# Performance work log

Hardware: AMD Instinct MI355X
Metric: run time of the kernel (lower is better)

The kernel has to match this reference:

```python
import jax, jax.numpy as jnp
import numpy as np

B, T, C = 2, 2048, 1024
H = 16
D = C // H  # head_dim = 64


def setup_inputs() -> dict:
    key = jax.random.key(0)
    k1, k2, k3, k4, k5 = jax.random.split(key, 5)
    s = 0.02
    return {
        "x": jax.random.normal(k1, (B, T, C), dtype=jnp.float32),
        "w_qkv": jax.random.normal(k2, (C, 3 * C), dtype=jnp.float32) * s,
        "b_qkv": jnp.zeros((3 * C,), dtype=jnp.float32),
        "w_proj": jax.random.normal(k3, (C, C), dtype=jnp.float32) * s,
        "b_proj": jnp.zeros((C,), dtype=jnp.float32),
    }


def reference(x, w_qkv, b_qkv, w_proj, b_proj):
    b, t, c = x.shape
    qkv = x @ w_qkv + b_qkv                      # [B,T,3C]
    q, k, v = jnp.split(qkv, 3, axis=-1)
    # [B,T,C] -> [B,H,T,D]
    q = q.reshape(b, t, H, D).transpose(0, 2, 1, 3)
    k = k.reshape(b, t, H, D).transpose(0, 2, 1, 3)
    v = v.reshape(b, t, H, D).transpose(0, 2, 1, 3)
    att = jnp.einsum("bhqd,bhkd->bhqk", q, k) / jnp.sqrt(jnp.float32(D))
    causal = jnp.tril(jnp.ones((t, t), dtype=bool))  # True where allowed
    att = jnp.where(causal, att, -jnp.inf)
    att = jax.nn.softmax(att, axis=-1)
    out = jnp.einsum("bhqk,bhkd->bhqd", att, v)      # [B,H,T,D]
    out = out.transpose(0, 2, 1, 3).reshape(b, t, c)
    return out @ w_proj + b_proj
```

## Files before the change

### kernel.cpp

```cpp
#include <hip/hip_runtime.h>
#include <hip/hip_bf16.h>
#include <math.h>
#include <stdint.h>

#define B_ 2
#define T_ 2048
#define C_ 1024
#define H_ 16
#define D_ 64

typedef __attribute__((ext_vector_type(8))) short bf16x8;
typedef __attribute__((ext_vector_type(4))) float f32x4;

__device__ inline short f2bf(float f) {
  __hip_bfloat16 h = __float2bfloat16(f);
  return *(short*)&h;
}

__device__ inline void async16(const void* g, void* l) {
  __builtin_amdgcn_global_load_lds(
      (const __attribute__((address_space(1))) uint32_t*)g,
      (__attribute__((address_space(3))) uint32_t*)l, 16, 0, 0);
}


__global__ __launch_bounds__(256) void prep(
    const float* __restrict__ X, const float* __restrict__ Wq,
    const float* __restrict__ Wp, short* __restrict__ Xb,
    short* __restrict__ Wqt, short* __restrict__ Wpt) {
  const int tid = threadIdx.x;
  const int blk = blockIdx.x;
  __shared__ short Ts[64][68];

  if (blk < 512) {
    int t = blk * 256 + tid;
    int m = t >> 5, g = t & 31;
    const float* src = X + (size_t)m * C_ + g * 32;
    short* dst = Xb + (size_t)m * C_ + g * 32;
    int xv = (m >> 1) & 3;
    short out[32];
#pragma unroll
    for (int ch = 0; ch < 4; ++ch) {
      int sc = ch ^ xv;
#pragma unroll
      for (int e = 0; e < 8; e += 4) {
        float4 v = *(const float4*)(src + sc * 8 + e);
        out[ch * 8 + e + 0] = f2bf(v.x);
        out[ch * 8 + e + 1] = f2bf(v.y);
        out[ch * 8 + e + 2] = f2bf(v.z);
        out[ch * 8 + e + 3] = f2bf(v.w);
      }
    }
#pragma unroll
    for (int q = 0; q < 4; ++q) *(uint4*)(dst + q * 8) = *(uint4*)(out + q * 8);
    return;
  }

  const float* W;
  short* Wt;
  int N, n0, k0;
  if (blk < 1280) {
    int i = blk - 512;
    W = Wq; Wt = Wqt; N = 3 * C_;
    n0 = (i % 48) * 64; k0 = (i / 48) * 64;
  } else {
    int i = blk - 1280;
    W = Wp; Wt = Wpt; N = C_;
    n0 = (i & 15) * 64; k0 = (i >> 4) * 64;
  }
  {
    int r = tid >> 2, c0 = (tid & 3) * 16;
    const float* src = W + (size_t)(k0 + r) * N + n0 + c0;
#pragma unroll
    for (int u = 0; u < 16; u += 4) {
      float4 v = *(const float4*)(src + u);
      Ts[r][c0 + u + 0] = f2bf(v.x);
      Ts[r][c0 + u + 1] = f2bf(v.y);
      Ts[r][c0 + u + 2] = f2bf(v.z);
      Ts[r][c0 + u + 3] = f2bf(v.w);
    }
  }
  __syncthreads();
#pragma unroll
  for (int p = 0; p < 2; ++p) {
    int n = (tid >> 3) + p * 32;
    int kc = tid & 7;
    int xv = ((n0 + n) >> 1) & 3;
    int ka = kc * 8;
    int dk = (ka & ~31) | ((((ka >> 3) & 3) ^ xv) << 3);
    short tmp[8];
#pragma unroll
    for (int u = 0; u < 8; ++u) tmp[u] = Ts[ka + u][n];
    *(uint4*)(Wt + (size_t)(n0 + n) * 1024 + k0 + dk) = *(uint4*)tmp;
  }
}

template <int N, int BN, bool QKV>
__global__ __launch_bounds__(256) void gemm_mfma(
    const short* __restrict__ A, const short* __restrict__ Bt,
    const float* __restrict__ bias, short* __restrict__ Qp,
    short* __restrict__ Kp, short* __restrict__ Vp, float* __restrict__ Cout) {
  constexpr int NJ = BN / 32;
  constexpr int BI = BN * 32;
  const int tid = threadIdx.x;
  const int wave = tid >> 6, lane = tid & 63;
  const int quad = lane >> 4, l16 = lane & 15;
  const int wm = wave >> 1, wn = wave & 1;
  const int m0 = blockIdx.y * 128, n0 = blockIdx.x * BN;

  __shared__ short As[2][4096];
  __shared__ short Bs[2][BI];

  const int srow = tid >> 2, skc = tid & 3;
  const size_t arow0 = (size_t)(m0 + srow) * 1024 + skc * 8;
  const size_t brow0 = (size_t)(n0 + srow) * 1024 + skc * 8;

  f32x4 acc[4][NJ] = {};

  const int xi = quad ^ ((l16 >> 1) & 3);
  int aoff[4], boff[NJ];
#pragma unroll
  for (int i = 0; i < 4; ++i) aoff[i] = (wm * 64 + i * 16 + l16) * 32 + xi * 8;
#pragma unroll
  for (int j = 0; j < NJ; ++j)
    boff[j] = (wn * (BN / 2) + j * 16 + l16) * 32 + xi * 8;

  for (int k0 = 0; k0 < 1024; k0 += 64) {
    __syncthreads();
#pragma unroll
    for (int f = 0; f < 2; ++f) {
      const int kf = k0 + f * 32;
      async16(A + arow0 + kf, &As[f][tid * 8]);
      async16(A + arow0 + (size_t)64 * 1024 + kf, &As[f][2048 + tid * 8]);
      async16(Bt + brow0 + kf, &Bs[f][tid * 8]);
      if (BN == 128)
        async16(Bt + brow0 + (size_t)64 * 1024 + kf, &Bs[f][2048 + tid * 8]);
    }
    __syncthreads();

#pragma unroll
    for (int f = 0; f < 2; ++f) {
      bf16x8 af[4], bfr[NJ];
#pragma unroll
      for (int i = 0; i < 4; ++i) af[i] = *(const bf16x8*)&As[f][aoff[i]];
#pragma unroll
      for (int j = 0; j < NJ; ++j) bfr[j] = *(const bf16x8*)&Bs[f][boff[j]];
#pragma unroll
      for (int i = 0; i < 4; ++i)
#pragma unroll
        for (int j = 0; j < NJ; ++j)
          acc[i][j] = __builtin_amdgcn_mfma_f32_16x16x32_bf16(
              af[i], bfr[j], acc[i][j], 0, 0, 0);
    }
  }

  float bj[NJ];
#pragma unroll
  for (int j = 0; j < NJ; ++j) bj[j] = bias[n0 + wn * (BN / 2) + j * 16 + l16];

  if (QKV) {
#pragma unroll
    for (int i = 0; i < 4; ++i) {
#pragma unroll
      for (int reg = 0; reg < 4; ++reg) {
        int m = m0 + wm * 64 + i * 16 + quad * 4 + reg;
        int b = m >> 11, t = m & (T_ - 1);
#pragma unroll
        for (int j = 0; j < NJ; ++j) {
          int n = n0 + wn * (BN / 2) + j * 16 + l16;
          float v = acc[i][j][reg] + bj[j];
          int sel = n >> 10, cc = n & (C_ - 1);
          int hh = cc >> 6, d = cc & 63;
          size_t base = (size_t)(b * H_ + hh) * 131072 + (size_t)(t >> 6) * 4096;
          if (sel == 0) {
            Qp[base + (d >> 3) * 512 + (t & 63) * 8 + (d & 7)] = f2bf(v * 0.125f);
          } else if (sel == 1) {
            Kp[base + (d >> 3) * 512 + (t & 63) * 8 + (d & 7)] = f2bf(v);
          } else {
            Vp[base + ((t & 63) >> 3) * 512 + d * 8 + (t & 7)] = f2bf(v);
          }
        }
      }
    }
  } else {
#pragma unroll
    for (int i = 0; i < 4; ++i) {
#pragma unroll
      for (int reg = 0; reg < 4; ++reg) {
        int m = m0 + wm * 64 + i * 16 + quad * 4 + reg;
#pragma unroll
        for (int j = 0; j < NJ; ++j) {
          int n = n0 + wn * (BN / 2) + j * 16 + l16;
          Cout[(size_t)m * N + n] = acc[i][j][reg] + bj[j];
        }
      }
    }
  }
}

__global__ __launch_bounds__(256, 4) void attn_kernel(
    const short* __restrict__ Qt, const short* __restrict__ Kt,
    const short* __restrict__ Vt, short* __restrict__ attb) {
  const int tid = threadIdx.x;
  const int wave = tid >> 6, lane = tid & 63;
  const int quad = lane >> 4, l16 = lane & 15;

  const int blk = blockIdx.x;
  const int bh = (blk >> 5) & 31;
  const int k2 = blk >> 8;
  int qtt = ((blk & 31) + 8 * (k2 >> 1)) & 31;
  const int qt = (k2 & 1) ? (31 - qtt) : qtt;
  const int h = bh & 15, b = bh >> 4;
  const int q0 = qt * 64;

  const short* Qg = Qt + (size_t)bh * 131072;
  const short* Kg = Kt + (size_t)bh * 131072;
  const short* Vg = Vt + (size_t)bh * 131072;

  __shared__ short Ks[2][4096];
  __shared__ short Vs[2][4096];
  __shared__ short Ps[4096];

  const int rowl = 16 * wave + l16;

  bf16x8 bq[2];
#pragma unroll
  for (int f = 0; f < 2; ++f)
    bq[f] = *(const bf16x8*)(Qg + (size_t)(qt * 8 + 4 * f + quad) * 512 +
                             rowl * 8);

  async16(Kg + tid * 8, &Ks[0][tid * 8]);
  async16(Kg + 2048 + tid * 8, &Ks[0][2048 + tid * 8]);
  async16(Vg + tid * 8, &Vs[0][tid * 8]);
  async16(Vg + 2048 + tid * 8, &Vs[0][2048 + tid * 8]);

  f32x4 oacc[4] = {};
  float lsum = 0.f;

  for (int kt = 0; kt <= qt; ++kt) {
    const int buf = kt & 1;
    __syncthreads();
    if (kt < qt) {
      const short* kp = Kg + (size_t)(kt + 1) * 4096;
      const short* vp = Vg + (size_t)(kt + 1) * 4096;
      async16(kp + tid * 8, &Ks[buf ^ 1][tid * 8]);
      async16(kp + 2048 + tid * 8, &Ks[buf ^ 1][2048 + tid * 8]);
      async16(vp + tid * 8, &Vs[buf ^ 1][tid * 8]);
      async16(vp + 2048 + tid * 8, &Vs[buf ^ 1][2048 + tid * 8]);
    }

    f32x4 sacc[4] = {};
#pragma unroll
    for (int c = 0; c < 4; ++c) {
#pragma unroll
      for (int f = 0; f < 2; ++f) {
        bf16x8 ak = *(const bf16x8*)&Ks[buf][((4 * f + quad) * 64 + 16 * c + l16) * 8];
        sacc[c] = __builtin_amdgcn_mfma_f32_16x16x32_bf16(ak, bq[f], sacc[c], 0, 0, 0);
      }
    }

    const bool diag = (kt == qt);
#pragma unroll
    for (int c = 0; c < 4; ++c) {
      short4 pk;
#pragma unroll
      for (int reg = 0; reg < 4; ++reg) {
        int keyl = 16 * c + 4 * quad + reg;
        float p = (diag && keyl > rowl) ? 0.f : __expf(sacc[c][reg]);
        lsum += p;
        ((short*)&pk)[reg] = f2bf(p);
      }
      *(short4*)&Ps[(2 * c + (quad >> 1)) * 512 + rowl * 8 + (quad & 1) * 4] = pk;
    }

    __asm__ volatile("s_waitcnt lgkmcnt(0)" ::: "memory");

    bf16x8 ap[2];
#pragma unroll
    for (int f = 0; f < 2; ++f)
      ap[f] = *(const bf16x8*)&Ps[(4 * f + quad) * 512 + rowl * 8];
#pragma unroll
    for (int n = 0; n < 4; ++n) {
#pragma unroll
      for (int f = 0; f < 2; ++f) {
        bf16x8 bv = *(const bf16x8*)&Vs[buf][((4 * f + quad) * 64 + 16 * n + l16) * 8];
        oacc[n] = __builtin_amdgcn_mfma_f32_16x16x32_bf16(ap[f], bv, oacc[n], 0, 0, 0);
      }
    }
  }

  lsum += __shfl_xor(lsum, 16);
  lsum += __shfl_xor(lsum, 32);
  float linv[4];
#pragma unroll
  for (int reg = 0; reg < 4; ++reg)
    linv[reg] = 1.0f / __shfl(lsum, 4 * quad + reg, 64);

#pragma unroll
  for (int reg = 0; reg < 4; ++reg) {
    const int row = q0 + 16 * wave + 4 * quad + reg;
    const int m = b * T_ + row;
    const int xv = (m >> 1) & 3;
#pragma unroll
    for (int n = 0; n < 4; ++n) {
      int c = h * 64 + 16 * n + l16;
      int cs = (c & ~31) | ((((c >> 3) & 3) ^ xv) << 3) | (c & 7);
      attb[(size_t)m * C_ + cs] = f2bf(oacc[n][reg] * linv[reg]);
    }
  }
}

extern "C" void kernel_launch(void* const* d_in, const int* in_sizes, int n_in,
                              void* d_out, int out_size, void* d_ws, size_t ws_size,
                              hipStream_t stream) {
  const float* x      = (const float*)d_in[0];
  const float* w_qkv  = (const float*)d_in[1];
  const float* b_qkv  = (const float*)d_in[2];
  const float* w_proj = (const float*)d_in[3];
  const float* b_proj = (const float*)d_in[4];
  float* out = (float*)d_out;

  const size_t per = (size_t)B_ * H_ * T_ * D_;
  short* Qp   = (short*)d_ws;
  short* Kp   = Qp + per;
  short* Vp   = Kp + per;
  short* attb = Vp + per;
  short* xb   = attb + per;
  short* wqt  = xb + per;
  short* wpt  = wqt + (size_t)3 * C_ * C_;

  prep<<<1536, 256, 0, stream>>>(x, w_qkv, w_proj, xb, wqt, wpt);

  gemm_mfma<3 * C_, 128, true><<<dim3(24, 32), 256, 0, stream>>>(
      xb, wqt, b_qkv, Qp, Kp, Vp, nullptr);

  attn_kernel<<<dim3(1024), 256, 0, stream>>>(Qp, Kp, Vp, attb);

  gemm_mfma<C_, 64, false><<<dim3(16, 32), 256, 0, stream>>>(
      attb, wpt, b_proj, nullptr, nullptr, nullptr, out);
}
```

Before: 177.1 us.

## Process two adjacent query tiles per attention block sharing K/V loads

Each attention block now handles two consecutive 64-row query tiles, so every K/V tile staged into LDS feeds both. The grid is halved and launch bounds relaxed to allow more registers. The softmax uses exp2 with log2(e) folded into the Q scale, and MFMA sections get raised wave priority. The X-to-bf16 conversion in prep is also rewritten so each thread loads one coalesced float4 per row. The cost is double the accumulator registers and lower occupancy, plus fewer blocks to balance across CUs.

New measurement: 179.4 us. Within noise of the previous version (+1.3%).

```diff
diff --git a/kernel.cpp b/kernel.cpp
--- a/kernel.cpp
+++ b/kernel.cpp
@@ -33,26 +33,19 @@
   __shared__ short Ts[64][68];
 
   if (blk < 512) {
-    int t = blk * 256 + tid;
-    int m = t >> 5, g = t & 31;
-    const float* src = X + (size_t)m * C_ + g * 32;
-    short* dst = Xb + (size_t)m * C_ + g * 32;
-    int xv = (m >> 1) & 3;
-    short out[32];
-#pragma unroll
-    for (int ch = 0; ch < 4; ++ch) {
-      int sc = ch ^ xv;
-#pragma unroll
-      for (int e = 0; e < 8; e += 4) {
-        float4 v = *(const float4*)(src + sc * 8 + e);
-        out[ch * 8 + e + 0] = f2bf(v.x);
-        out[ch * 8 + e + 1] = f2bf(v.y);
-        out[ch * 8 + e + 2] = f2bf(v.z);
-        out[ch * 8 + e + 3] = f2bf(v.w);
-      }
-    }
-#pragma unroll
-    for (int q = 0; q < 4; ++q) *(uint4*)(dst + q * 8) = *(uint4*)(out + q * 8);
+    const int g = tid >> 3;
+    const int sub = tid & 7;
+    const int sc = sub >> 1;
+    const int e4 = (sub & 1) * 4;
+#pragma unroll
+    for (int pass = 0; pass < 8; ++pass) {
+      const int m = blk * 8 + pass;
+      float4 v = *(const float4*)(X + (size_t)m * C_ + tid * 4);
+      const int xv = (m >> 1) & 3;
+      short o[4] = {f2bf(v.x), f2bf(v.y), f2bf(v.z), f2bf(v.w)};
+      *(uint2*)(Xb + (size_t)m * C_ + g * 32 + ((sc ^ xv) << 3) + e4) =
+          *(uint2*)o;
+    }
     return;
   }
 
@@ -173,7 +166,8 @@
           int hh = cc >> 6, d = cc & 63;
           size_t base = (size_t)(b * H_ + hh) * 131072 + (size_t)(t >> 6) * 4096;
           if (sel == 0) {
-            Qp[base + (d >> 3) * 512 + (t & 63) * 8 + (d & 7)] = f2bf(v * 0.125f);
+            Qp[base + (d >> 3) * 512 + (t & 63) * 8 + (d & 7)] =
+                f2bf(v * 0.18033688011112042f);
           } else if (sel == 1) {
             Kp[base + (d >> 3) * 512 + (t & 63) * 8 + (d & 7)] = f2bf(v);
           } else {
@@ -198,7 +192,7 @@
   }
 }
 
-__global__ __launch_bounds__(256, 4) void attn_kernel(
+__global__ __launch_bounds__(256, 2) void attn_kernel(
     const short* __restrict__ Qt, const short* __restrict__ Kt,
     const short* __restrict__ Vt, short* __restrict__ attb) {
   const int tid = threadIdx.x;
@@ -206,12 +200,11 @@
   const int quad = lane >> 4, l16 = lane & 15;
 
   const int blk = blockIdx.x;
-  const int bh = (blk >> 5) & 31;
-  const int k2 = blk >> 8;
-  int qtt = ((blk & 31) + 8 * (k2 >> 1)) & 31;
-  const int qt = (k2 & 1) ? (31 - qtt) : qtt;
+  const int bh = blk & 31;
+  const int i = blk >> 5;
+  const int pj = (i < 8) ? (15 - i) : (i - 8);
+  const int NT = 2 * pj + 2;
   const int h = bh & 15, b = bh >> 4;
-  const int q0 = qt * 64;
 
   const short* Qg = Qt + (size_t)bh * 131072;
   const short* Kg = Kt + (size_t)bh * 131072;
@@ -219,93 +212,181 @@
 
   __shared__ short Ks[2][4096];
   __shared__ short Vs[2][4096];
-  __shared__ short Ps[4096];
+  __shared__ short Ps[2][4096];
 
   const int rowl = 16 * wave + l16;
 
-  bf16x8 bq[2];
-#pragma unroll
-  for (int f = 0; f < 2; ++f)
-    bq[f] = *(const bf16x8*)(Qg + (size_t)(qt * 8 + 4 * f + quad) * 512 +
-                             rowl * 8);
+  bf16x8 bq[2][2];
+#pragma unroll
+  for (int g = 0; g < 2; ++g)
+#pragma unroll
+    for (int f = 0; f < 2; ++f)
+      bq[g][f] = *(const bf16x8*)(Qg +
+                 (size_t)((2 * pj + g) * 8 + 4 * f + quad) * 512 + rowl * 8);
 
   async16(Kg + tid * 8, &Ks[0][tid * 8]);
   async16(Kg + 2048 + tid * 8, &Ks[0][2048 + tid * 8]);
   async16(Vg + tid * 8, &Vs[0][tid * 8]);
   async16(Vg + 2048 + tid * 8, &Vs[0][2048 + tid * 8]);
 
-  f32x4 oacc[4] = {};
-  float lsum = 0.f;
-
-  for (int kt = 0; kt <= qt; ++kt) {
+  f32x4 oacc[4][2] = {};
+  float lsum[2] = {0.f, 0.f};
+
+  auto stage_next = [&](int kt) {
+    const int dst = (kt + 1) & 1;
+    const short* kp = Kg + (size_t)(kt + 1) * 4096;
+    const short* vp = Vg + (size_t)(kt + 1) * 4096;
+    async16(kp + tid * 8, &Ks[dst][tid * 8]);
+    async16(kp + 2048 + tid * 8, &Ks[dst][2048 + tid * 8]);
+    async16(vp + tid * 8, &Vs[dst][tid * 8]);
+    async16(vp + 2048 + tid * 8, &Vs[dst][2048 + tid * 8]);
+  };
+
+  auto qkt2 = [&](int buf, f32x4 (&sacc)[4][2]) {
+    __builtin_amdgcn_s_setprio(1);
+#pragma unroll
+    for (int c = 0; c < 4; ++c) {
+#pragma unroll
+      for (int f = 0; f < 2; ++f) {
+        bf16x8 ak =
+            *(const bf16x8*)&Ks[buf][((4 * f + quad) * 64 + 16 * c + l16) * 8];
+        sacc[c][0] = __builtin_amdgcn_mfma_f32_16x16x32_bf16(
+            ak, bq[0][f], sacc[c][0], 0, 0, 0);
+        sacc[c][1] = __builtin_amdgcn_mfma_f32_16x16x32_bf16(
+            ak, bq[1][f], sacc[c][1], 0, 0, 0);
+      }
+    }
+    __builtin_amdgcn_s_setprio(0);
+  };
+
+  auto smax = [&](f32x4 (&sacc)[4][2], int g, bool mask) {
+#pragma unroll
+    for (int c = 0; c < 4; ++c) {
+      short4 pk;
+#pragma unroll
+      for (int reg = 0; reg < 4; ++reg) {
+        int keyl = 16 * c + 4 * quad + reg;
+        float p = (mask && keyl > rowl)
+                      ? 0.f
+                      : __builtin_amdgcn_exp2f(sacc[c][g][reg]);
+        lsum[g] += p;
+        ((short*)&pk)[reg] = f2bf(p);
+      }
+      *(short4*)&Ps[g][(2 * c + (quad >> 1)) * 512 + rowl * 8 + (quad & 1) * 4] =
+          pk;
+    }
+  };
+
+  auto pv2 = [&](int buf) {
+    __asm__ volatile("s_waitcnt lgkmcnt(0)" ::: "memory");
+    bf16x8 ap[2][2];
+#pragma unroll
+    for (int f = 0; f < 2; ++f) {
+      ap[0][f] = *(const bf16x8*)&Ps[0][(4 * f + quad) * 512 + rowl * 8];
+      ap[1][f] = *(const bf16x8*)&Ps[1][(4 * f + quad) * 512 + rowl * 8];
+    }
+    __builtin_amdgcn_s_setprio(1);
+#pragma unroll
+    for (int n = 0; n < 4; ++n) {
+#pragma unroll
+      for (int f = 0; f < 2; ++f) {
+        bf16x8 bv =
+            *(const bf16x8*)&Vs[buf][((4 * f + quad) * 64 + 16 * n + l16) * 8];
+        oacc[n][0] = __builtin_amdgcn_mfma_f32_16x16x32_bf16(
+            ap[0][f], bv, oacc[n][0], 0, 0, 0);
+        oacc[n][1] = __builtin_amdgcn_mfma_f32_16x16x32_bf16(
+            ap[1][f], bv, oacc[n][1], 0, 0, 0);
+      }
+    }
+    __builtin_amdgcn_s_setprio(0);
+  };
+
+  for (int kt = 0; kt < NT - 2; ++kt) {
     const int buf = kt & 1;
     __syncthreads();
-    if (kt < qt) {
-      const short* kp = Kg + (size_t)(kt + 1) * 4096;
-      const short* vp = Vg + (size_t)(kt + 1) * 4096;
-      async16(kp + tid * 8, &Ks[buf ^ 1][tid * 8]);
-      async16(kp + 2048 + tid * 8, &Ks[buf ^ 1][2048 + tid * 8]);
-      async16(vp + tid * 8, &Vs[buf ^ 1][tid * 8]);
-      async16(vp + 2048 + tid * 8, &Vs[buf ^ 1][2048 + tid * 8]);
-    }
-
-    f32x4 sacc[4] = {};
-#pragma unroll
-    for (int c = 0; c < 4; ++c) {
+    stage_next(kt);
+    f32x4 sacc[4][2] = {};
+    qkt2(buf, sacc);
+    smax(sacc, 0, false);
+    smax(sacc, 1, false);
+    pv2(buf);
+  }
+  {
+    const int kt = NT - 2, buf = kt & 1;
+    __syncthreads();
+    stage_next(kt);
+    f32x4 sacc[4][2] = {};
+    qkt2(buf, sacc);
+    smax(sacc, 0, true);
+    smax(sacc, 1, false);
+    pv2(buf);
+  }
+  {
+    const int buf = (NT - 1) & 1;
+    __syncthreads();
+    f32x4 sacc1[4] = {};
+    __builtin_amdgcn_s_setprio(1);
+#pragma unroll
+    for (int c = 0; c < 4; ++c)
 #pragma unroll
       for (int f = 0; f < 2; ++f) {
-        bf16x8 ak = *(const bf16x8*)&Ks[buf][((4 * f + quad) * 64 + 16 * c + l16) * 8];
-        sacc[c] = __builtin_amdgcn_mfma_f32_16x16x32_bf16(ak, bq[f], sacc[c], 0, 0, 0);
-      }
-    }
-
-    const bool diag = (kt == qt);
+        bf16x8 ak =
+            *(const bf16x8*)&Ks[buf][((4 * f + quad) * 64 + 16 * c + l16) * 8];
+        sacc1[c] = __builtin_amdgcn_mfma_f32_16x16x32_bf16(
+            ak, bq[1][f], sacc1[c], 0, 0, 0);
+      }
+    __builtin_amdgcn_s_setprio(0);
 #pragma unroll
     for (int c = 0; c < 4; ++c) {
       short4 pk;
 #pragma unroll
       for (int reg = 0; reg < 4; ++reg) {
         int keyl = 16 * c + 4 * quad + reg;
-        float p = (diag && keyl > rowl) ? 0.f : __expf(sacc[c][reg]);
-        lsum += p;
+        float p = (keyl > rowl) ? 0.f : __builtin_amdgcn_exp2f(sacc1[c][reg]);
+        lsum[1] += p;
         ((short*)&pk)[reg] = f2bf(p);
       }
-      *(short4*)&Ps[(2 * c + (quad >> 1)) * 512 + rowl * 8 + (quad & 1) * 4] = pk;
-    }
-
+      *(short4*)&Ps[1][(2 * c + (quad >> 1)) * 512 + rowl * 8 + (quad & 1) * 4] =
+          pk;
+    }
     __asm__ volatile("s_waitcnt lgkmcnt(0)" ::: "memory");
-
-    bf16x8 ap[2];
+    bf16x8 ap1[2];
 #pragma unroll
     for (int f = 0; f < 2; ++f)
-      ap[f] = *(const bf16x8*)&Ps[(4 * f + quad) * 512 + rowl * 8];
-#pragma unroll
-    for (int n = 0; n < 4; ++n) {
+      ap1[f] = *(const bf16x8*)&Ps[1][(4 * f + quad) * 512 + rowl * 8];
+    __builtin_amdgcn_s_setprio(1);
+#pragma unroll
+    for (int n = 0; n < 4; ++n)
 #pragma unroll
       for (int f = 0; f < 2; ++f) {
-        bf16x8 bv = *(const bf16x8*)&Vs[buf][((4 * f + quad) * 64 + 16 * n + l16) * 8];
-        oacc[n] = __builtin_amdgcn_mfma_f32_16x16x32_bf16(ap[f], bv, oacc[n], 0, 0, 0);
-      }
-    }
-  }
-
-  lsum += __shfl_xor(lsum, 16);
-  lsum += __shfl_xor(lsum, 32);
-  float linv[4];
-#pragma unroll
-  for (int reg = 0; reg < 4; ++reg)
-    linv[reg] = 1.0f / __shfl(lsum, 4 * quad + reg, 64);
-
-#pragma unroll
-  for (int reg = 0; reg < 4; ++reg) {
-    const int row = q0 + 16 * wave + 4 * quad + reg;
-    const int m = b * T_ + row;
-    const int xv = (m >> 1) & 3;
-#pragma unroll
-    for (int n = 0; n < 4; ++n) {
-      int c = h * 64 + 16 * n + l16;
-      int cs = (c & ~31) | ((((c >> 3) & 3) ^ xv) << 3) | (c & 7);
-      attb[(size_t)m * C_ + cs] = f2bf(oacc[n][reg] * linv[reg]);
+        bf16x8 bv =
+            *(const bf16x8*)&Vs[buf][((4 * f + quad) * 64 + 16 * n + l16) * 8];
+        oacc[n][1] = __builtin_amdgcn_mfma_f32_16x16x32_bf16(
+            ap1[f], bv, oacc[n][1], 0, 0, 0);
+      }
+    __builtin_amdgcn_s_setprio(0);
+  }
+
+#pragma unroll
+  for (int g = 0; g < 2; ++g) {
+    float ls = lsum[g];
+    ls += __shfl_xor(ls, 16);
+    ls += __shfl_xor(ls, 32);
+    float linv[4];
+#pragma unroll
+    for (int reg = 0; reg < 4; ++reg)
+      linv[reg] = 1.0f / __shfl(ls, 4 * quad + reg, 64);
+#pragma unroll
+    for (int reg = 0; reg < 4; ++reg) {
+      const int row = (2 * pj + g) * 64 + 16 * wave + 4 * quad + reg;
+      const int m = b * T_ + row;
+      const int xv = (m >> 1) & 3;
+#pragma unroll
+      for (int n = 0; n < 4; ++n) {
+        int c = h * 64 + 16 * n + l16;
+        int cs = (c & ~31) | ((((c >> 3) & 3) ^ xv) << 3) | (c & 7);
+        attb[(size_t)m * C_ + cs] = f2bf(oacc[n][g][reg] * linv[reg]);
+      }
     }
   }
 }
@@ -334,7 +415,7 @@
   gemm_mfma<3 * C_, 128, true><<<dim3(24, 32), 256, 0, stream>>>(
       xb, wqt, b_qkv, Qp, Kp, Vp, nullptr);
 
-  attn_kernel<<<dim3(1024), 256, 0, stream>>>(Qp, Kp, Vp, attb);
+  attn_kernel<<<dim3(512), 256, 0, stream>>>(Qp, Kp, Vp, attb);
 
   gemm_mfma<C_, 64, false><<<dim3(16, 32), 256, 0, stream>>>(
       attb, wpt, b_proj, nullptr, nullptr, nullptr, out);
```
